# Performance work log

Measured on AMD Instinct MI355X. Metric: run time of the kernel, lower is better.

The kernel has to match this reference:

```python
import jax, jax.numpy as jnp
import numpy as np

NUM_GROUPS = 32
EPS = 1e-6


def group_norm(x, gamma, beta):
    # x: [b, c, h, w]
    b, c, h, w = x.shape
    xg = x.reshape(b, NUM_GROUPS, c // NUM_GROUPS, h, w)
    mean = xg.mean(axis=(2, 3, 4), keepdims=True)
    var = xg.var(axis=(2, 3, 4), keepdims=True)
    xn = ((xg - mean) * jax.lax.rsqrt(var + EPS)).reshape(b, c, h, w)
    return xn * gamma[None, :, None, None] + beta[None, :, None, None]


def conv1x1(x, w, bias):
    # 1x1 conv == channel-mixing matmul. x: [b,c,h,w], w: [co,ci]
    y = jnp.einsum('bchw,oc->bohw', x, w)
    return y + bias[None, :, None, None]


def setup_inputs() -> dict:
    key = jax.random.key(0)
    ks = jax.random.split(key, 10)
    B, C, H, W = 4, 512, 64, 64
    s = 1.0 / np.sqrt(C)
    inp = {
        'x': jax.random.normal(ks[0], (B, C, H, W), jnp.float32),
        'gamma': jnp.ones((C,), jnp.float32),
        'beta': jnp.zeros((C,), jnp.float32),
        'wq': jax.random.normal(ks[1], (C, C), jnp.float32) * s,
        'bq': jnp.zeros((C,), jnp.float32),
        'wk': jax.random.normal(ks[2], (C, C), jnp.float32) * s,
        'bk': jnp.zeros((C,), jnp.float32),
        'wv': jax.random.normal(ks[3], (C, C), jnp.float32) * s,
        'bv': jnp.zeros((C,), jnp.float32),
        'wo': jax.random.normal(ks[4], (C, C), jnp.float32) * s,
        'bo': jnp.zeros((C,), jnp.float32),
    }
    return inp


def reference(x, gamma, beta, wq, bq, wk, bk, wv, bv, wo, bo):
    b, c, h, w = x.shape
    h_ = group_norm(x, gamma, beta)
    q = conv1x1(h_, wq, bq).reshape(b, c, h * w)  # [b,c,n]
    k = conv1x1(h_, wk, bk).reshape(b, c, h * w)
    v = conv1x1(h_, wv, bv).reshape(b, c, h * w)
    scale = jnp.asarray(c, x.dtype) ** -0.5
    # scores: [b, n, n] = q^T k
    scores = jnp.einsum('bcn,bcm->bnm', q, k) * scale
    attn = jax.nn.softmax(scores, axis=2)
    # out: [b, c, n] = v @ attn^T  (h_[i] = sum_j attn[i,j] v[j])
    out = jnp.einsum('bnm,bcm->bcn', attn, v).reshape(b, c, h, w)
    out = conv1x1(out, wo, bo)
    return x + out
```

## Files before the change

### kernel.cpp

```cpp
#include <hip/hip_runtime.h>

typedef __bf16 bf16x8 __attribute__((ext_vector_type(8)));
typedef float f32x4 __attribute__((ext_vector_type(4)));
typedef unsigned short u16;

__device__ __forceinline__ u16 f2bf(float f) {
  unsigned int u = __builtin_bit_cast(unsigned int, f);
  u += 0x7fff + ((u >> 16) & 1);
  return (u16)(u >> 16);
}
__device__ __forceinline__ float bf2f(u16 s) {
  unsigned int u = ((unsigned int)s) << 16;
  return __builtin_bit_cast(float, u);
}
__device__ __forceinline__ void unp8(uint4 u, float* f) {
  f[0] = bf2f(u.x & 0xffff); f[1] = bf2f(u.x >> 16);
  f[2] = bf2f(u.y & 0xffff); f[3] = bf2f(u.y >> 16);
  f[4] = bf2f(u.z & 0xffff); f[5] = bf2f(u.z >> 16);
  f[6] = bf2f(u.w & 0xffff); f[7] = bf2f(u.w >> 16);
}
__device__ __forceinline__ uint4 pk8(const float* f) {
  uint4 u;
  u.x = (unsigned)f2bf(f[0]) | ((unsigned)f2bf(f[1]) << 16);
  u.y = (unsigned)f2bf(f[2]) | ((unsigned)f2bf(f[3]) << 16);
  u.z = (unsigned)f2bf(f[4]) | ((unsigned)f2bf(f[5]) << 16);
  u.w = (unsigned)f2bf(f[6]) | ((unsigned)f2bf(f[7]) << 16);
  return u;
}

__device__ __forceinline__ void gl_lds16(const u16* g, u16* l) {
  __builtin_amdgcn_global_load_lds(
      (const __attribute__((address_space(1))) void*)g,
      (__attribute__((address_space(3))) void*)l, 16, 0, 0);
}

__global__ __launch_bounds__(512, 2) void gemm_nt256(
    const u16* __restrict__ A, int lda, unsigned long long sA,
    const u16* __restrict__ Bt, int ldb, unsigned long long sB,
    u16* __restrict__ Cout, int ldc, unsigned long long sC,
    unsigned long long sSplit, int K, float alpha, int tn,
    const float* __restrict__ bias_col, float* __restrict__ psum) {
  __shared__ u16 lds[2][4][8192];
  __shared__ float part[4][256];

  const int t = threadIdx.x;
  const int lane = t & 63;
  const int w = t >> 6;
  const int bz = blockIdx.z;
  A  += (size_t)bz * sA + (size_t)blockIdx.y * K;
  Bt += (size_t)bz * sB + (size_t)blockIdx.y * K;
  Cout += (size_t)blockIdx.y * sSplit;

  const int nwg = gridDim.x;
  const int flat = blockIdx.x;
  const int wg = (flat & 7) * (nwg >> 3) + (flat >> 3);
  const int m0 = (wg / tn) * 256;
  const int n0 = (wg % tn) * 256;

  const int NKT = K >> 6;

  const int sr = lane >> 3;
  const int sc = ((lane & 7) ^ sr) * 8;
  const u16* gA = A  + (size_t)(m0 + w * 16 + sr) * lda + sc;
  const u16* gB = Bt + (size_t)(n0 + w * 16 + sr) * ldb + sc;
  const size_t a128 = (size_t)128 * lda, b128 = (size_t)128 * ldb;
  const size_t a8 = (size_t)8 * lda, b8 = (size_t)8 * ldb;
  const int lws = w * 1024;

  auto stage = [&](int slot, int region, int kt) {
    kt = kt < NKT ? kt : NKT - 1;
    u16* l = &lds[slot][region][lws];
    if (region < 2) {
      const u16* g = gA + (region ? a128 : 0) + (size_t)kt * 64;
      gl_lds16(g, l);
      gl_lds16(g + a8, l + 512);
    } else {
      const u16* g = gB + (region == 3 ? b128 : 0) + (size_t)kt * 64;
      gl_lds16(g, l);
      gl_lds16(g + b8, l + 512);
    }
  };

  const int wr = w >> 2, wc = w & 3;
  const int fr = lane & 15, kg = lane >> 4;
  const int frx = (fr & 7) << 4;

  f32x4 acc[8][4] = {};
  bf16x8 af[4][2], bq[2][2];

#define LDA_(s, qm)                                                            \
  {                                                                            \
    const u16* Ab = &lds[s][0][0];                                             \
    _Pragma("unroll") for (int m = 0; m < 4; ++m) {                            \
      const int R = wr * 128 + (qm) * 64 + m * 16 + fr;                        \
      _Pragma("unroll") for (int kk = 0; kk < 2; ++kk)                         \
          af[m][kk] = *reinterpret_cast<const bf16x8*>(                        \
              Ab + R * 64 + (((kk * 64 + kg * 16) ^ frx) >> 1));               \
    }                                                                          \
  }
#define LDB_(s, qn)                                                            \
  {                                                                            \
    const u16* Bb = &lds[s][2][0];                                             \
    _Pragma("unroll") for (int n = 0; n < 2; ++n) {                            \
      const int R = wc * 64 + (qn) * 32 + n * 16 + fr;                         \
      _Pragma("unroll") for (int kk = 0; kk < 2; ++kk)                         \
          bq[n][kk] = *reinterpret_cast<const bf16x8*>(                        \
              Bb + R * 64 + (((kk * 64 + kg * 16) ^ frx) >> 1));               \
    }                                                                          \
  }
#define PH(s, qm, qn, DOA, DOB, ss, rr, kt, VM)                                \
  {                                                                            \
    if (DOA) LDA_(s, qm)                                                       \
    if (DOB) LDB_(s, qn)                                                       \
    stage(ss, rr, kt);                                                         \
    __builtin_amdgcn_s_barrier();                                              \
    asm volatile("s_waitcnt lgkmcnt(0)" ::: "memory");                         \
    __builtin_amdgcn_s_setprio(1);                                             \
    _Pragma("unroll") for (int kk = 0; kk < 2; ++kk)                           \
    _Pragma("unroll") for (int m = 0; m < 4; ++m)                              \
    _Pragma("unroll") for (int n = 0; n < 2; ++n)                              \
        acc[(qm)*4 + m][(qn)*2 + n] = __builtin_amdgcn_mfma_f32_16x16x32_bf16( \
            af[m][kk], bq[n][kk], acc[(qm)*4 + m][(qn)*2 + n], 0, 0, 0);       \
    __builtin_amdgcn_s_setprio(0);                                             \
    if (VM) asm volatile("s_waitcnt vmcnt(2)" ::: "memory");                   \
    __builtin_amdgcn_s_barrier();                                              \
  }

  stage(0, 0, 0); stage(0, 1, 0); stage(0, 2, 0); stage(0, 3, 0);
  stage(1, 0, 1);
  asm volatile("s_waitcnt vmcnt(2)" ::: "memory");
  __builtin_amdgcn_s_barrier();

  for (int j = 0; j < (NKT >> 1); ++j) {
    const int k1 = 2 * j + 1, k2 = 2 * j + 2, k3 = 2 * j + 3;
    PH(0, 0, 0, 1, 1, 1, 1, k1, 0)
    PH(0, 0, 1, 0, 1, 1, 2, k1, 0)
    PH(0, 1, 1, 1, 0, 1, 3, k1, 0)
    PH(0, 1, 0, 0, 1, 0, 0, k2, 1)
    PH(1, 0, 0, 1, 1, 0, 1, k2, 0)
    PH(1, 0, 1, 0, 1, 0, 2, k2, 0)
    PH(1, 1, 1, 1, 0, 0, 3, k2, 0)
    PH(1, 1, 0, 0, 1, 1, 0, k3, 1)
  }
#undef PH
#undef LDB_
#undef LDA_

  __syncthreads();
  u16* cs = &lds[0][0][0];
  if (psum) {
#pragma unroll
    for (int a = 0; a < 8; ++a) {
      const int row = wr * 128 + a * 16 + (kg << 2);
      float sr_[4] = {0.f, 0.f, 0.f, 0.f};
#pragma unroll
      for (int b = 0; b < 4; ++b) {
        const int col = wc * 64 + b * 16 + fr;
#pragma unroll
        for (int r = 0; r < 4; ++r) {
          const float p = exp2f(acc[a][b][r] * alpha);
          sr_[r] += p;
          cs[(row + r) * 256 + col] = f2bf(p);
        }
      }
#pragma unroll
      for (int r = 0; r < 4; ++r) {
#pragma unroll
        for (int msk = 1; msk < 16; msk <<= 1)
          sr_[r] += __shfl_xor(sr_[r], msk);
        if (fr == 0) part[wc][row + r] = sr_[r];
      }
    }
  } else {
#pragma unroll
    for (int a = 0; a < 8; ++a)
#pragma unroll
      for (int b = 0; b < 4; ++b) {
        const int col = wc * 64 + b * 16 + fr;
        const float bc = bias_col ? bias_col[n0 + col] : 0.0f;
        const int row = wr * 128 + a * 16 + (kg << 2);
#pragma unroll
        for (int r = 0; r < 4; ++r)
          cs[(row + r) * 256 + col] = f2bf(acc[a][b][r] * alpha + bc);
      }
  }
  __syncthreads();
  const size_t cbs = (size_t)bz * sC;
#pragma unroll
  for (int it = 0; it < 16; ++it) {
    const int off = (it * 512 + t) * 8;
    const int row = off >> 8, col = off & 255;
    *reinterpret_cast<uint4*>(&Cout[cbs + (size_t)(m0 + row) * ldc + (n0 + col)]) =
        *reinterpret_cast<const uint4*>(&cs[off]);
  }
  if (psum && t < 256) {
    const int Mrows = (nwg / tn) << 8;
    psum[((size_t)bz * tn + (n0 >> 8)) * Mrows + m0 + t] =
        part[0][t] + part[1][t] + part[2][t] + part[3][t];
  }
}

template <bool OUT_F32>
__global__ __launch_bounds__(256) void gemm_nt(
    const u16* __restrict__ A, int lda, unsigned long long sA,
    const u16* __restrict__ Bt, int ldb, unsigned long long sB,
    void* __restrict__ Cout, int ldc, unsigned long long sC,
    int K, float alpha,
    const float* __restrict__ bias_row, const float* __restrict__ bias_col,
    const float* __restrict__ residual, unsigned long long sRes) {
  __shared__ u16 lds[128 * 128];
  u16* As = lds;
  u16* Bs = lds + 8192;

  const int t = threadIdx.x;
  const int bz = blockIdx.z;
  A  += (size_t)bz * sA;
  Bt += (size_t)bz * sB;
  const int m0 = blockIdx.x * 128;
  const int n0 = blockIdx.y * 128;

  const int lane = t & 63;
  const int w = t >> 6;

  const int srow = w * 32 + (lane >> 3);
  const int scol = (lane & 7) * 8;
  const u16* gA = A  + (size_t)(m0 + srow) * lda + scol;
  const u16* gB = Bt + (size_t)(n0 + srow) * ldb + scol;
  u16* lA = As + w * 2048;
  u16* lB = Bs + w * 2048;

  f32x4 acc[4][4] = {};
  const int wm = (w >> 1) * 64;
  const int wn = (w & 1) * 64;
  const int fr = lane & 15;
  const int kg = lane >> 4;

  for (int k0 = 0; k0 < K; k0 += 64) {
    __syncthreads();
#pragma unroll
    for (int i = 0; i < 4; ++i) {
      gl_lds16(gA + (size_t)(i * 8) * lda + k0, lA + i * 512);
      gl_lds16(gB + (size_t)(i * 8) * ldb + k0, lB + i * 512);
    }
    __syncthreads();

#pragma unroll
    for (int kk = 0; kk < 2; ++kk) {
      bf16x8 af[4], bfr[4];
#pragma unroll
      for (int m = 0; m < 4; ++m)
        af[m] = *reinterpret_cast<const bf16x8*>(
            &As[(wm + m * 16 + fr) * 64 + kk * 32 + kg * 8]);
#pragma unroll
      for (int n = 0; n < 4; ++n)
        bfr[n] = *reinterpret_cast<const bf16x8*>(
            &Bs[(wn + n * 16 + fr) * 64 + kk * 32 + kg * 8]);
#pragma unroll
      for (int m = 0; m < 4; ++m)
#pragma unroll
        for (int n = 0; n < 4; ++n)
          acc[m][n] = __builtin_amdgcn_mfma_f32_16x16x32_bf16(af[m], bfr[n], acc[m][n], 0, 0, 0);
    }
  }

  const size_t cbase = (size_t)bz * sC;
  const size_t rbase = (size_t)bz * sRes;
  const int rq = kg * 4;

  if (OUT_F32) {
    float* Cf = reinterpret_cast<float*>(Cout);
    float* lf = reinterpret_cast<float*>(lds);
#pragma unroll
    for (int h = 0; h < 2; ++h) {
      __syncthreads();
      if ((wm >> 6) == h) {
#pragma unroll
        for (int m = 0; m < 4; ++m)
#pragma unroll
          for (int n = 0; n < 4; ++n) {
            const float bc = bias_col ? bias_col[n0 + wn + n * 16 + fr] : 0.0f;
#pragma unroll
            for (int r = 0; r < 4; ++r)
              lf[(m * 16 + rq + r) * 128 + (wn + n * 16 + fr)] =
                  acc[m][n][r] * alpha + bc;
          }
      }
      __syncthreads();
#pragma unroll
      for (int it = 0; it < 8; ++it) {
        const int off = (it * 256 + t) * 4;
        const int row = off >> 7, col = off & 127;
        const int grow = m0 + h * 64 + row, gcol = n0 + col;
        float4 v = *reinterpret_cast<const float4*>(&lf[off]);
        if (bias_row) {
          const float br = bias_row[grow];
          v.x += br; v.y += br; v.z += br; v.w += br;
        }
        if (residual) {
          const float4 rx = *reinterpret_cast<const float4*>(
              &residual[rbase + (size_t)grow * ldc + gcol]);
          v.x += rx.x; v.y += rx.y; v.z += rx.z; v.w += rx.w;
        }
        *reinterpret_cast<float4*>(&Cf[cbase + (size_t)grow * ldc + gcol]) = v;
      }
    }
  } else {
    __syncthreads();
#pragma unroll
    for (int m = 0; m < 4; ++m) {
#pragma unroll
      for (int n = 0; n < 4; ++n) {
        const int gcol = n0 + wn + n * 16 + fr;
        const float bc = bias_col ? bias_col[gcol] : 0.0f;
#pragma unroll
        for (int r = 0; r < 4; ++r) {
          const int grow = m0 + wm + m * 16 + rq + r;
          float v = acc[m][n][r] * alpha + bc;
          if (bias_row) v += bias_row[grow];
          lds[(wm + m * 16 + rq + r) * 128 + (wn + n * 16 + fr)] = f2bf(v);
        }
      }
    }
    __syncthreads();
    u16* Cb = reinterpret_cast<u16*>(Cout);
#pragma unroll
    for (int j = 0; j < 8; ++j) {
      const int off = (j * 256 + t) * 8;
      const int row = off >> 7, col = off & 127;
      *reinterpret_cast<uint4*>(&Cb[cbase + (size_t)(m0 + row) * ldc + (n0 + col)]) =
          *reinterpret_cast<const uint4*>(&lds[off]);
    }
  }
}

__global__ __launch_bounds__(256) void groupnorm_k(
    const float* __restrict__ x, const float* __restrict__ gamma,
    const float* __restrict__ beta, u16* __restrict__ h_t, int C, int N) {
  const int g = blockIdx.x;
  const int b = blockIdx.y;
  const int t = threadIdx.x;
  const float* xb = x + ((size_t)b * C + g * 16) * N;

  float s = 0.f, q = 0.f;
  for (int c = 0; c < 16; ++c) {
    const float4* xr = reinterpret_cast<const float4*>(xb + (size_t)c * N);
    for (int j = t; j < N / 4; j += 256) {
      float4 v = xr[j];
      s += v.x + v.y + v.z + v.w;
      q += v.x * v.x + v.y * v.y + v.z * v.z + v.w * v.w;
    }
  }
#pragma unroll
  for (int o = 32; o > 0; o >>= 1) { s += __shfl_down(s, o); q += __shfl_down(q, o); }
  __shared__ float rs[4], rqs[4], stats[2];
  const int lane = t & 63, wid = t >> 6;
  if (lane == 0) { rs[wid] = s; rqs[wid] = q; }
  __syncthreads();
  if (t == 0) {
    float S = rs[0] + rs[1] + rs[2] + rs[3];
    float Q = rqs[0] + rqs[1] + rqs[2] + rqs[3];
    const float inv = 1.0f / (16.0f * (float)N);
    float mean = S * inv;
    float var = Q * inv - mean * mean;
    stats[0] = mean;
    stats[1] = rsqrtf(var + 1e-6f);
  }
  __syncthreads();
  const float mean = stats[0], rstd = stats[1];

  float gm[16], bt[16];
#pragma unroll
  for (int c = 0; c < 16; ++c) {
    gm[c] = gamma[g * 16 + c] * rstd;
    bt[c] = beta[g * 16 + c] - mean * gm[c];
  }
  u16* ho = h_t + (size_t)b * N * C + g * 16;
  for (int n = t; n < N; n += 256) {
    union { u16 us[16]; uint4 v4[2]; } pk;
#pragma unroll
    for (int c = 0; c < 16; ++c) {
      float v = xb[(size_t)c * N + n];
      pk.us[c] = f2bf(v * gm[c] + bt[c]);
    }
    uint4* dst = reinterpret_cast<uint4*>(ho + (size_t)n * C);
    dst[0] = pk.v4[0];
    dst[1] = pk.v4[1];
  }
}

__global__ __launch_bounds__(256) void wcvt(const float* __restrict__ src,
                                            u16* __restrict__ dst, int n) {
  const int i = (blockIdx.x * 256 + threadIdx.x) * 8;
  if (i >= n) return;
  const float4* s4 = reinterpret_cast<const float4*>(src + i);
  float4 a = s4[0], b = s4[1];
  float f[8] = {a.x, a.y, a.z, a.w, b.x, b.y, b.z, b.w};
  *reinterpret_cast<uint4*>(dst + i) = pk8(f);
}

__global__ __launch_bounds__(256) void bcat2(const float* __restrict__ a,
                                             const float* __restrict__ b,
                                             float* __restrict__ o, int n) {
  const int i = blockIdx.x * 256 + threadIdx.x;
  if (i < n) o[i] = a[i];
  else if (i < 2 * n) o[i] = b[i - n];
}

__global__ __launch_bounds__(256) void sumred(const float* __restrict__ psum,
                                              float* __restrict__ invl,
                                              int nt, int rows, int total) {
  const int i = blockIdx.x * 256 + threadIdx.x;
  if (i >= total) return;
  const int b = i / rows, n = i - b * rows;
  const float* p = psum + (size_t)b * nt * rows + n;
  float s = 0.f;
  for (int c = 0; c < nt; ++c) s += p[(size_t)c * rows];
  invl[i] = 1.0f / s;
}

__global__ __launch_bounds__(256) void reduce_pv(const u16* __restrict__ p,
                                                 const float* __restrict__ invl,
                                                 u16* __restrict__ o, int n) {
  const int i = (blockIdx.x * 256 + threadIdx.x) * 8;
  if (i >= n) return;
  const float il = invl[i >> 9];
  uint4 a = *reinterpret_cast<const uint4*>(p + i);
  uint4 b = *reinterpret_cast<const uint4*>(p + n + i);
  float fa[8], fb[8];
  unp8(a, fa); unp8(b, fb);
#pragma unroll
  for (int j = 0; j < 8; ++j) fa[j] = (fa[j] + fb[j]) * il;
  *reinterpret_cast<uint4*>(o + i) = pk8(fa);
}

__global__ __launch_bounds__(256) void scale_o(u16* __restrict__ o,
                                               const float* __restrict__ invl,
                                               int n) {
  const int i = (blockIdx.x * 256 + threadIdx.x) * 8;
  if (i >= n) return;
  const float il = invl[i >> 9];
  uint4 a = *reinterpret_cast<const uint4*>(o + i);
  float fa[8];
  unp8(a, fa);
#pragma unroll
  for (int j = 0; j < 8; ++j) fa[j] *= il;
  *reinterpret_cast<uint4*>(o + i) = pk8(fa);
}

extern "C" void kernel_launch(void* const* d_in, const int* in_sizes, int n_in,
                              void* d_out, int out_size, void* d_ws, size_t ws_size,
                              hipStream_t stream) {
  const float* x     = (const float*)d_in[0];
  const float* gamma = (const float*)d_in[1];
  const float* beta  = (const float*)d_in[2];
  const float* wq    = (const float*)d_in[3];
  const float* bq    = (const float*)d_in[4];
  const float* wk    = (const float*)d_in[5];
  const float* bk    = (const float*)d_in[6];
  const float* wv    = (const float*)d_in[7];
  const float* bv    = (const float*)d_in[8];
  const float* wo    = (const float*)d_in[9];
  const float* bo    = (const float*)d_in[10];

  const int B = 4, C = 512, N = 4096;
  const size_t NC = (size_t)N * C;
  const size_t NN = (size_t)N * N;
  const size_t CC = (size_t)C * C;

  char* ws = (char*)d_ws;
  size_t off = 0;
  auto alloc = [&](size_t bytes) {
    size_t r = off;
    off = (off + bytes + 255) & ~(size_t)255;
    return r;
  };
  u16* wq_b = (u16*)(ws + alloc(CC * 2));
  u16* wk_b = (u16*)(ws + alloc(CC * 2));
  u16* wv_b = (u16*)(ws + alloc(CC * 2));
  u16* wo_b = (u16*)(ws + alloc(CC * 2));
  float* bqk = (float*)(ws + alloc(1024 * 4));
  u16* h_t  = (u16*)(ws + alloc(B * NC * 2));
  u16* qk_t = (u16*)(ws + alloc(B * N * 1024 * 2));
  u16* v_cn = (u16*)(ws + alloc(B * NC * 2));
  u16* o_t  = (u16*)(ws + alloc(B * NC * 2));
  float* psum = (float*)(ws + alloc((size_t)B * 16 * N * 4));
  float* invl = (float*)(ws + alloc((size_t)B * N * 4));
  const size_t base_need = off;

  int s_batched = 0;
  u16* S;
  if (ws_size >= base_need + B * NN * 2) {
    S = (u16*)(ws + alloc(B * NN * 2));
    s_batched = 1;
  } else {
    S = (u16*)(ws + alloc(NN * 2));
  }
  u16* o_part = qk_t;

  wcvt<<<dim3(CC / 2048), 256, 0, stream>>>(wq, wq_b, (int)CC);
  wcvt<<<dim3(CC / 2048), 256, 0, stream>>>(wk, wk_b, (int)CC);
  wcvt<<<dim3(CC / 2048), 256, 0, stream>>>(wv, wv_b, (int)CC);
  wcvt<<<dim3(CC / 2048), 256, 0, stream>>>(wo, wo_b, (int)CC);
  bcat2<<<dim3(4), 256, 0, stream>>>(bq, bk, bqk, C);

  groupnorm_k<<<dim3(32, B), 256, 0, stream>>>(x, gamma, beta, h_t, C, N);

  gemm_nt256<<<dim3((N / 256) * (1024 / 256), 1, B), 512, 0, stream>>>(
      h_t, C, NC, wq_b, C, 0, qk_t, 1024, (unsigned long long)N * 1024, 0,
      C, 1.0f, 1024 / 256, bqk, nullptr);
  dim3 gv(C / 128, N / 128, B);
  gemm_nt<false><<<gv, 256, 0, stream>>>(wv_b, C, 0, h_t, C, NC, v_cn, N, NC,
                                         C, 1.0f, bv, nullptr, nullptr, 0);

  const float c1 = 0.06376694387439652f;
  if (s_batched) {
    gemm_nt256<<<dim3((N / 256) * (N / 256), 1, B), 512, 0, stream>>>(
        qk_t, 1024, (unsigned long long)N * 1024, qk_t + 512, 1024,
        (unsigned long long)N * 1024, S, N, NN, 0, C, c1, N / 256, nullptr, psum);
    sumred<<<dim3(B * N / 256), 256, 0, stream>>>(psum, invl, 16, N, B * N);
    gemm_nt256<<<dim3((N / 256) * (C / 256), 2, B), 512, 0, stream>>>(
        S, N, NN, v_cn, N, NC, o_part, C, NC, (unsigned long long)B * NC,
        N / 2, 1.0f, C / 256, nullptr, nullptr);
    reduce_pv<<<dim3((int)(B * NC / 2048)), 256, 0, stream>>>(
        o_part, invl, o_t, (int)(B * NC));
  } else {
    for (int b = 0; b < B; ++b) {
      gemm_nt256<<<dim3((N / 256) * (N / 256), 1, 1), 512, 0, stream>>>(
          qk_t + (size_t)b * N * 1024, 1024, 0, qk_t + (size_t)b * N * 1024 + 512,
          1024, 0, S, N, 0, 0, C, c1, N / 256, nullptr, psum + (size_t)b * 16 * N);
      gemm_nt256<<<dim3((N / 256) * (C / 256), 1, 1), 512, 0, stream>>>(
          S, N, 0, v_cn + (size_t)b * NC, N, 0, o_t + (size_t)b * NC, C, 0, 0,
          N, 1.0f, C / 256, nullptr, nullptr);
    }
    sumred<<<dim3(B * N / 256), 256, 0, stream>>>(psum, invl, 16, N, B * N);
    scale_o<<<dim3((int)(B * NC / 2048)), 256, 0, stream>>>(o_t, invl, (int)(B * NC));
  }

  dim3 gf(C / 128, N / 128, B);
  gemm_nt<true><<<gf, 256, 0, stream>>>(wo_b, C, 0, o_t, C, NC, d_out, N, NC,
                                        C, 1.0f, bo, nullptr, x, NC);
}
```

Measured before the change: 334.4 us.

## Compute softmax row sums via MFMA with ones vector inside PV GEMM

Moves the softmax denominator computation out of the QK^T epilogue, which used shuffle reductions and a shared partial array, into the PV GEMM. There, waves with wc==0 issue extra MFMAs multiplying the bf16 probability tiles by a ones vector. The kernel is templated on a mode so each use compiles only its own epilogue, and the psum buffer shrinks from 16 to 2 partials per row. This cuts epilogue work and psum traffic in the score GEMM, but adds MFMA work on a quarter of the waves in PV. The sums now come from the bf16-rounded probabilities rather than the fp32 values, which changes numerics slightly.

Measured after the change: 317.6 us. 5.0% less time.

```diff
diff --git a/kernel.cpp b/kernel.cpp
--- a/kernel.cpp
+++ b/kernel.cpp
@@ -34,6 +34,7 @@
       (__attribute__((address_space(3))) void*)l, 16, 0, 0);
 }
 
+template <int MODE>
 __global__ __launch_bounds__(512, 2) void gemm_nt256(
     const u16* __restrict__ A, int lda, unsigned long long sA,
     const u16* __restrict__ Bt, int ldb, unsigned long long sB,
@@ -41,7 +42,6 @@
     unsigned long long sSplit, int K, float alpha, int tn,
     const float* __restrict__ bias_col, float* __restrict__ psum) {
   __shared__ u16 lds[2][4][8192];
-  __shared__ float part[4][256];
 
   const int t = threadIdx.x;
   const int lane = t & 63;
@@ -86,7 +86,12 @@
   const int frx = (fr & 7) << 4;
 
   f32x4 acc[8][4] = {};
+  f32x4 sacc[8] = {};
   bf16x8 af[4][2], bq[2][2];
+  union { u16 u[8]; bf16x8 v; } ou;
+#pragma unroll
+  for (int i = 0; i < 8; ++i) ou.u[i] = 0x3F80;
+  const bf16x8 onesb = ou.v;
 
 #define LDA_(s, qm)                                                            \
   {                                                                            \
@@ -121,6 +126,12 @@
     _Pragma("unroll") for (int n = 0; n < 2; ++n)                              \
         acc[(qm)*4 + m][(qn)*2 + n] = __builtin_amdgcn_mfma_f32_16x16x32_bf16( \
             af[m][kk], bq[n][kk], acc[(qm)*4 + m][(qn)*2 + n], 0, 0, 0);       \
+    if (MODE == 2 && (DOA) && wc == 0) {                                       \
+      _Pragma("unroll") for (int kk = 0; kk < 2; ++kk)                         \
+      _Pragma("unroll") for (int m = 0; m < 4; ++m)                            \
+          sacc[(qm)*4 + m] = __builtin_amdgcn_mfma_f32_16x16x32_bf16(          \
+              af[m][kk], onesb, sacc[(qm)*4 + m], 0, 0, 0);                    \
+    }                                                                          \
     __builtin_amdgcn_s_setprio(0);                                             \
     if (VM) asm volatile("s_waitcnt vmcnt(2)" ::: "memory");                   \
     __builtin_amdgcn_s_barrier();                                              \
@@ -148,41 +159,22 @@
 
   __syncthreads();
   u16* cs = &lds[0][0][0];
-  if (psum) {
-#pragma unroll
-    for (int a = 0; a < 8; ++a) {
-      const int row = wr * 128 + a * 16 + (kg << 2);
-      float sr_[4] = {0.f, 0.f, 0.f, 0.f};
-#pragma unroll
-      for (int b = 0; b < 4; ++b) {
-        const int col = wc * 64 + b * 16 + fr;
-#pragma unroll
-        for (int r = 0; r < 4; ++r) {
-          const float p = exp2f(acc[a][b][r] * alpha);
-          sr_[r] += p;
-          cs[(row + r) * 256 + col] = f2bf(p);
-        }
+#pragma unroll
+  for (int a = 0; a < 8; ++a) {
+    const int row = wr * 128 + a * 16 + (kg << 2);
+#pragma unroll
+    for (int b = 0; b < 4; ++b) {
+      const int col = wc * 64 + b * 16 + fr;
+      float bc = 0.0f;
+      if (MODE == 0 && bias_col) bc = bias_col[n0 + col];
+#pragma unroll
+      for (int r = 0; r < 4; ++r) {
+        float v;
+        if (MODE == 1) v = exp2f(acc[a][b][r] * alpha);
+        else v = acc[a][b][r] * alpha + bc;
+        cs[(row + r) * 256 + col] = f2bf(v);
       }
-#pragma unroll
-      for (int r = 0; r < 4; ++r) {
-#pragma unroll
-        for (int msk = 1; msk < 16; msk <<= 1)
-          sr_[r] += __shfl_xor(sr_[r], msk);
-        if (fr == 0) part[wc][row + r] = sr_[r];
-      }
-    }
-  } else {
-#pragma unroll
-    for (int a = 0; a < 8; ++a)
-#pragma unroll
-      for (int b = 0; b < 4; ++b) {
-        const int col = wc * 64 + b * 16 + fr;
-        const float bc = bias_col ? bias_col[n0 + col] : 0.0f;
-        const int row = wr * 128 + a * 16 + (kg << 2);
-#pragma unroll
-        for (int r = 0; r < 4; ++r)
-          cs[(row + r) * 256 + col] = f2bf(acc[a][b][r] * alpha + bc);
-      }
+    }
   }
   __syncthreads();
   const size_t cbs = (size_t)bz * sC;
@@ -193,10 +185,16 @@
     *reinterpret_cast<uint4*>(&Cout[cbs + (size_t)(m0 + row) * ldc + (n0 + col)]) =
         *reinterpret_cast<const uint4*>(&cs[off]);
   }
-  if (psum && t < 256) {
+  if (MODE == 2 && psum && wc == 0 && fr == 0) {
     const int Mrows = (nwg / tn) << 8;
-    psum[((size_t)bz * tn + (n0 >> 8)) * Mrows + m0 + t] =
-        part[0][t] + part[1][t] + part[2][t] + part[3][t];
+    float* pp = psum + ((size_t)bz * gridDim.y + blockIdx.y) * Mrows + m0;
+#pragma unroll
+    for (int q = 0; q < 2; ++q)
+#pragma unroll
+      for (int m = 0; m < 4; ++m)
+#pragma unroll
+        for (int r = 0; r < 4; ++r)
+          pp[wr * 128 + q * 64 + m * 16 + (kg << 2) + r] = sacc[q * 4 + m][r];
   }
 }
 
@@ -483,7 +481,7 @@
   u16* qk_t = (u16*)(ws + alloc(B * N * 1024 * 2));
   u16* v_cn = (u16*)(ws + alloc(B * NC * 2));
   u16* o_t  = (u16*)(ws + alloc(B * NC * 2));
-  float* psum = (float*)(ws + alloc((size_t)B * 16 * N * 4));
+  float* psum = (float*)(ws + alloc((size_t)B * 2 * N * 4));
   float* invl = (float*)(ws + alloc((size_t)B * N * 4));
   const size_t base_need = off;
 
@@ -505,7 +503,7 @@
 
   groupnorm_k<<<dim3(32, B), 256, 0, stream>>>(x, gamma, beta, h_t, C, N);
 
-  gemm_nt256<<<dim3((N / 256) * (1024 / 256), 1, B), 512, 0, stream>>>(
+  gemm_nt256<0><<<dim3((N / 256) * (1024 / 256), 1, B), 512, 0, stream>>>(
       h_t, C, NC, wq_b, C, 0, qk_t, 1024, (unsigned long long)N * 1024, 0,
       C, 1.0f, 1024 / 256, bqk, nullptr);
   dim3 gv(C / 128, N / 128, B);
@@ -514,25 +512,25 @@
 
   const float c1 = 0.06376694387439652f;
   if (s_batched) {
-    gemm_nt256<<<dim3((N / 256) * (N / 256), 1, B), 512, 0, stream>>>(
+    gemm_nt256<1><<<dim3((N / 256) * (N / 256), 1, B), 512, 0, stream>>>(
         qk_t, 1024, (unsigned long long)N * 1024, qk_t + 512, 1024,
-        (unsigned long long)N * 1024, S, N, NN, 0, C, c1, N / 256, nullptr, psum);
-    sumred<<<dim3(B * N / 256), 256, 0, stream>>>(psum, invl, 16, N, B * N);
-    gemm_nt256<<<dim3((N / 256) * (C / 256), 2, B), 512, 0, stream>>>(
+        (unsigned long long)N * 1024, S, N, NN, 0, C, c1, N / 256, nullptr, nullptr);
+    gemm_nt256<2><<<dim3((N / 256) * (C / 256), 2, B), 512, 0, stream>>>(
         S, N, NN, v_cn, N, NC, o_part, C, NC, (unsigned long long)B * NC,
-        N / 2, 1.0f, C / 256, nullptr, nullptr);
+        N / 2, 1.0f, C / 256, nullptr, psum);
+    sumred<<<dim3(B * N / 256), 256, 0, stream>>>(psum, invl, 2, N, B * N);
     reduce_pv<<<dim3((int)(B * NC / 2048)), 256, 0, stream>>>(
         o_part, invl, o_t, (int)(B * NC));
   } else {
     for (int b = 0; b < B; ++b) {
-      gemm_nt256<<<dim3((N / 256) * (N / 256), 1, 1), 512, 0, stream>>>(
+      gemm_nt256<1><<<dim3((N / 256) * (N / 256), 1, 1), 512, 0, stream>>>(
           qk_t + (size_t)b * N * 1024, 1024, 0, qk_t + (size_t)b * N * 1024 + 512,
-          1024, 0, S, N, 0, 0, C, c1, N / 256, nullptr, psum + (size_t)b * 16 * N);
-      gemm_nt256<<<dim3((N / 256) * (C / 256), 1, 1), 512, 0, stream>>>(
+          1024, 0, S, N, 0, 0, C, c1, N / 256, nullptr, nullptr);
+      gemm_nt256<2><<<dim3((N / 256) * (C / 256), 1, 1), 512, 0, stream>>>(
           S, N, 0, v_cn + (size_t)b * NC, N, 0, o_t + (size_t)b * NC, C, 0, 0,
-          N, 1.0f, C / 256, nullptr, nullptr);
-    }
-    sumred<<<dim3(B * N / 256), 256, 0, stream>>>(psum, invl, 16, N, B * N);
+          N, 1.0f, C / 256, nullptr, psum + (size_t)b * N);
+    }
+    sumred<<<dim3(B * N / 256), 256, 0, stream>>>(psum, invl, 1, N, B * N);
     scale_o<<<dim3((int)(B * NC / 2048)), 256, 0, stream>>>(o_t, invl, (int)(B * NC));
   }
 
```
